# Kernel tuning notes

Hardware: AMD Instinct MI355X
Metric: run time of the kernel (lower is better)

## Reference

```python
import jax, jax.numpy as jnp
import numpy as np

B, S, D, H, FF = 2, 2048, 1024, 16, 4096
DK = D // H
EPS = 1e-5


def setup_inputs() -> dict:
    key = jax.random.key(0)
    ks = jax.random.split(key, 16)
    sd = 0.02
    return {
        "x": jax.random.normal(ks[0], (B, S, D), jnp.float32),
        "mask": jnp.ones((B, 1, 1, S), jnp.int32),
        "wq_w": jax.random.normal(ks[1], (D, D), jnp.float32) * sd,
        "wq_b": jnp.zeros((D,), jnp.float32),
        "wk_w": jax.random.normal(ks[2], (D, D), jnp.float32) * sd,
        "wk_b": jnp.zeros((D,), jnp.float32),
        "wv_w": jax.random.normal(ks[3], (D, D), jnp.float32) * sd,
        "wv_b": jnp.zeros((D,), jnp.float32),
        "wo_w": jax.random.normal(ks[4], (D, D), jnp.float32) * sd,
        "wo_b": jnp.zeros((D,), jnp.float32),
        "ff1_w": jax.random.normal(ks[5], (FF, D), jnp.float32) * sd,
        "ff1_b": jnp.zeros((FF,), jnp.float32),
        "ff2_w": jax.random.normal(ks[6], (D, FF), jnp.float32) * sd,
        "ff2_b": jnp.zeros((D,), jnp.float32),
        "ln1_a": jnp.ones((D,), jnp.float32),
        "ln1_b": jnp.zeros((D,), jnp.float32),
        "ln2_a": jnp.ones((D,), jnp.float32),
        "ln2_b": jnp.zeros((D,), jnp.float32),
    }


def _layernorm(x, alpha, beta):
    # Matches torch module: std is unbiased (ddof=1), divides by (std + eps)
    mean = jnp.mean(x, -1, keepdims=True)
    std = jnp.std(x, -1, keepdims=True, ddof=1)
    return (x - mean) / (std + EPS) * alpha + beta


def _mha(x, mask, wq_w, wq_b, wk_w, wk_b, wv_w, wv_b, wo_w, wo_b):
    q = (x @ wq_w.T + wq_b).reshape(B, S, H, DK).transpose(0, 2, 1, 3)
    k = (x @ wk_w.T + wk_b).reshape(B, S, H, DK).transpose(0, 2, 1, 3)
    v = (x @ wv_w.T + wv_b).reshape(B, S, H, DK).transpose(0, 2, 1, 3)
    scores = jnp.einsum('bhqd,bhkd->bhqk', q, k) / jnp.sqrt(jnp.float32(DK))
    scores = jnp.where(mask == 0, -jnp.inf, scores)
    attn = jax.nn.softmax(scores, axis=-1)
    out = jnp.einsum('bhqk,bhkd->bhqd', attn, v)
    out = out.transpose(0, 2, 1, 3).reshape(B, S, D)
    return out @ wo_w.T + wo_b


def reference(x, mask, wq_w, wq_b, wk_w, wk_b, wv_w, wv_b, wo_w, wo_b,
              ff1_w, ff1_b, ff2_w, ff2_b, ln1_a, ln1_b, ln2_a, ln2_b):
    # Residual 1: pre-norm + self-attention (dropout = 0)
    h = _layernorm(x, ln1_a, ln1_b)
    x = x + _mha(h, mask, wq_w, wq_b, wk_w, wk_b, wv_w, wv_b, wo_w, wo_b)
    # Residual 2: pre-norm + FFN
    h = _layernorm(x, ln2_a, ln2_b)
    ff = jax.nn.relu(h @ ff1_w.T + ff1_b) @ ff2_w.T + ff2_b
    return x + ff
```

## Files before the change

### kernel.cpp

```cpp
#include <hip/hip_runtime.h>
#include <hip/hip_bf16.h>
#include <stdint.h>

#define B_   2
#define S_   2048
#define D_   1024
#define H_   16
#define FF_  4096
#define TOK  4096
#define EPS_ 1e-5f
#define SC2  0.18033688f

typedef __attribute__((ext_vector_type(8))) short short8;
typedef __attribute__((ext_vector_type(4))) short short4_t;
typedef __attribute__((ext_vector_type(4))) float float4_t;

__device__ __forceinline__ short f2bf(float f) {
  union { float f; uint32_t u; } v; v.f = f;
  uint32_t r = v.u + 0x7fffu + ((v.u >> 16) & 1u);
  return (short)(r >> 16);
}

__device__ __forceinline__ float bf2f(short s) {
  union { uint32_t u; float f; } v; v.u = ((uint32_t)(uint16_t)s) << 16; return v.f;
}

__device__ __forceinline__ uint32_t pkbf(float a, float b) {
  __hip_bfloat162 h = __float22bfloat162_rn(make_float2(a, b));
  union { __hip_bfloat162 h; uint32_t u; } c; c.h = h; return c.u;
}

__device__ __forceinline__ void gload_lds16(const void* g, void* l) {
  __builtin_amdgcn_global_load_lds(
      (const __attribute__((address_space(1))) void*)g,
      (__attribute__((address_space(3))) void*)l, 16, 0, 0);
}

__global__ __launch_bounds__(256) void prep_kernel(
    const float* __restrict__ x, const float* __restrict__ ln1a,
    const float* __restrict__ ln1b, short* __restrict__ h1,
    const int* __restrict__ m, float* __restrict__ maskb, int* __restrict__ flags,
    const float* __restrict__ wq, const float* __restrict__ wk,
    const float* __restrict__ wv, const float* __restrict__ wo,
    const float* __restrict__ f1, const float* __restrict__ f2,
    short* __restrict__ wout)
{
  const int blk = blockIdx.x;
  const int tid = threadIdx.x;
  if (blk < TOK) {
    const int row = blk;
    const float4_t v = *(const float4_t*)(x + (size_t)row * D_ + tid * 4);
    float s  = v[0] + v[1] + v[2] + v[3];
    float ss = v[0]*v[0] + v[1]*v[1] + v[2]*v[2] + v[3]*v[3];
    #pragma unroll
    for (int mm = 1; mm < 64; mm <<= 1) { s += __shfl_xor(s, mm); ss += __shfl_xor(ss, mm); }
    __shared__ float red[8];
    const int wave = tid >> 6, lane = tid & 63;
    if (lane == 0) { red[wave] = s; red[4 + wave] = ss; }
    __syncthreads();
    s  = red[0] + red[1] + red[2] + red[3];
    ss = red[4] + red[5] + red[6] + red[7];
    const float mean = s * (1.0f / D_);
    float var = (ss - (float)D_ * mean * mean) * (1.0f / (D_ - 1));
    var = fmaxf(var, 0.0f);
    const float inv = 1.0f / (sqrtf(var) + EPS_);
    short4_t o;
    #pragma unroll
    for (int j = 0; j < 4; j++) {
      float a = ln1a[tid*4 + j], bb = ln1b[tid*4 + j];
      o[j] = f2bf((v[j] - mean) * inv * a + bb);
    }
    *(short4_t*)(h1 + (size_t)row * D_ + tid * 4) = o;
  } else if (blk < TOK + 16) {
    const int i = (blk - TOK) * 256 + tid;
    const int mv = m[i];
    maskb[i] = mv ? 0.0f : -1e30f;
    unsigned long long bal = __ballot(mv == 0);
    if ((tid & 63) == 0) flags[i >> 6] = (bal != 0ull) ? 1 : 0;
  } else {
    const int n4 = (12 << 20) / 4;
    const int nb = gridDim.x - TOK - 16;
    int idx = (blk - TOK - 16) * 256 + tid;
    const int stride = nb * 256;
    for (int j4 = idx; j4 < n4; j4 += stride) {
      const int j = j4 * 4;
      const int seg = j >> 20;
      const float* src; int off;
      if (seg < 4)      { src = (seg == 0) ? wq : (seg == 1) ? wk : (seg == 2) ? wv : wo;
                          off = j & ((1 << 20) - 1); }
      else if (seg < 8) { src = f1; off = j - (4 << 20); }
      else              { src = f2; off = j - (8 << 20); }
      float4_t v = *(const float4_t*)(src + off);
      short4_t o = { f2bf(v[0]), f2bf(v[1]), f2bf(v[2]), f2bf(v[3]) };
      *(short4_t*)(wout + j) = o;
    }
  }
}

__global__ void combine3_kernel(const float* __restrict__ x2,
                                const short* __restrict__ pA,
                                const short* __restrict__ pB,
                                float* __restrict__ out, const float* __restrict__ bias,
                                int n) {
  int idx = blockIdx.x * blockDim.x + threadIdx.x;
  int stride = gridDim.x * blockDim.x;
  for (int j = idx * 4; j < n; j += stride * 4) {
    float4_t a  = *(const float4_t*)(x2 + j);
    float4_t c  = *(const float4_t*)(out + j);
    float4_t bb = *(const float4_t*)(bias + (j & (D_ - 1)));
    short4_t q0 = *(const short4_t*)(pA + j);
    short4_t q1 = *(const short4_t*)(pA + (4u << 20) + j);
    short4_t q2 = *(const short4_t*)(pB + j);
    float4_t o;
    #pragma unroll
    for (int e = 0; e < 4; e++)
      o[e] = a[e] + c[e] + bb[e] + bf2f(q0[e]) + bf2f(q1[e]) + bf2f(q2[e]);
    *(float4_t*)(out + j) = o;
  }
}

__global__ __launch_bounds__(256) void ln_kernel(
    const float* __restrict__ x, const float* __restrict__ alpha,
    const float* __restrict__ beta, short* __restrict__ out)
{
  const int row = blockIdx.x;
  const int tid = threadIdx.x;
  const float4_t v = *(const float4_t*)(x + (size_t)row * D_ + tid * 4);
  float s  = v[0] + v[1] + v[2] + v[3];
  float ss = v[0]*v[0] + v[1]*v[1] + v[2]*v[2] + v[3]*v[3];
  #pragma unroll
  for (int m = 1; m < 64; m <<= 1) { s += __shfl_xor(s, m); ss += __shfl_xor(ss, m); }
  __shared__ float red[8];
  const int wave = tid >> 6, lane = tid & 63;
  if (lane == 0) { red[wave] = s; red[4 + wave] = ss; }
  __syncthreads();
  s  = red[0] + red[1] + red[2] + red[3];
  ss = red[4] + red[5] + red[6] + red[7];
  const float mean = s * (1.0f / D_);
  float var = (ss - (float)D_ * mean * mean) * (1.0f / (D_ - 1));
  var = fmaxf(var, 0.0f);
  const float inv = 1.0f / (sqrtf(var) + EPS_);
  short4_t o;
  #pragma unroll
  for (int j = 0; j < 4; j++) {
    float a = alpha[tid*4 + j], bb = beta[tid*4 + j];
    o[j] = f2bf((v[j] - mean) * inv * a + bb);
  }
  *(short4_t*)(out + (size_t)row * D_ + tid * 4) = o;
}

template<int EPI, int BN>
__global__ __launch_bounds__(256) void gemm_bt(
    const short* __restrict__ A, const short* __restrict__ Bm,
    void* __restrict__ Cout, void* __restrict__ Cout2,
    const float* __restrict__ bias, const float* __restrict__ res,
    int N, int K, int lda, int ldb)
{
  __shared__ __align__(16) short As[2][128][32];
  __shared__ __align__(16) short Bs[2][BN][32];

  const int tid  = threadIdx.x;
  const int wave = tid >> 6, lane = tid & 63;
  const int l15  = lane & 15, l4 = lane >> 4;

  const int gx = gridDim.x, gy = gridDim.y;
  int bid = (blockIdx.z * gy + blockIdx.y) * gx + blockIdx.x;
  const int q8 = (gx * gy * gridDim.z) >> 3;
  bid = (bid & 7) * q8 + (bid >> 3);
  const int n0 = (bid % gx) * BN;
  const int m0 = ((bid / gx) % gy) * 128;
  const int zi = bid / (gx * gy);
  const int koff = zi * K;

  constexpr int MI = (BN == 128) ? 4 : 2;
  const int rb = (BN == 128) ? (wave >> 1) * 64 : wave * 32;
  const int cb = (BN == 128) ? (wave & 1) * 64 : 0;

  float4_t acc[MI][4] = {};

  const int scol = (lane & 3) * 8;
  const short* gA0 = A + (size_t)(m0 + wave*32 + (lane >> 2)) * lda + koff + scol;
  const short* gA1 = gA0 + (size_t)16 * lda;
  const short* gB0;
  const short* gB1 = nullptr;
  if (BN == 128) {
    gB0 = Bm + (size_t)(n0 + wave*32 + (lane >> 2)) * ldb + koff + scol;
    gB1 = gB0 + (size_t)16 * ldb;
  } else {
    gB0 = Bm + (size_t)(n0 + wave*16 + (lane >> 2)) * ldb + koff + scol;
  }

  gload_lds16(gA0, &As[0][wave*32][0]);
  gload_lds16(gA1, &As[0][wave*32 + 16][0]);
  if (BN == 128) {
    gload_lds16(gB0, &Bs[0][wave*32][0]);
    gload_lds16(gB1, &Bs[0][wave*32 + 16][0]);
  } else {
    gload_lds16(gB0, &Bs[0][wave*16][0]);
  }

  for (int k0 = 0; k0 < K; k0 += 32) {
    const int cur = (k0 >> 5) & 1;
    __syncthreads();
    if (k0 + 32 < K) {
      gload_lds16(gA0 + k0 + 32, &As[cur^1][wave*32][0]);
      gload_lds16(gA1 + k0 + 32, &As[cur^1][wave*32 + 16][0]);
      if (BN == 128) {
        gload_lds16(gB0 + k0 + 32, &Bs[cur^1][wave*32][0]);
        gload_lds16(gB1 + k0 + 32, &Bs[cur^1][wave*32 + 16][0]);
      } else {
        gload_lds16(gB0 + k0 + 32, &Bs[cur^1][wave*16][0]);
      }
    }
    short8 af[MI], bf[4];
    #pragma unroll
    for (int i = 0; i < MI; i++)
      af[i] = *(const short8*)&As[cur][rb + i*16 + l15][l4*8];
    #pragma unroll
    for (int i = 0; i < 4; i++)
      bf[i] = *(const short8*)&Bs[cur][cb + i*16 + l15][l4*8];
    #pragma unroll
    for (int mi = 0; mi < MI; mi++)
      #pragma unroll
      for (int ni = 0; ni < 4; ni++)
        acc[mi][ni] = __builtin_amdgcn_mfma_f32_16x16x32_bf16(af[mi], bf[ni], acc[mi][ni], 0, 0, 0);
  }

  const int crow0 = m0 + rb + l4*4;
  const int ccol0 = n0 + cb + l15;
  #pragma unroll
  for (int mi = 0; mi < MI; mi++) {
    #pragma unroll
    for (int ni = 0; ni < 4; ni++) {
      const int col = ccol0 + ni*16;
      const float bc = bias[col];
      #pragma unroll
      for (int r = 0; r < 4; r++) {
        const int row = crow0 + mi*16 + r;
        ((float*)Cout)[(size_t)row * N + col] =
            res[(size_t)row * N + col] + acc[mi][ni][r] + bc;
      }
    }
  }
}

#define G256_DECLS                                                            \
  const int tid = threadIdx.x;                                                \
  const int w = tid >> 6, lane = tid & 63;                                    \
  const int wm = w >> 2, wn = w & 3;                                          \
  const int l15 = lane & 15, l4 = lane >> 4;                                  \
  const int srow = w*8 + (lane >> 3);                                         \
  const int schk = ((lane & 7) ^ (((lane >> 5) & 1) << 1)) * 8;               \
  const int rswz = (l4 ^ (((l15 >> 2) & 1) << 1)) * 8;                        \
  const int aoff = (wm*128 + l15) * 64 + rswz;                                \
  const int boff = (wn*64  + l15) * 64 + rswz;

#define G256_STG(buf_, koff_, LDA_) do {                                      \
    short* da = lds + (buf_)*16384 + w*512;                                   \
    short* db = lds + 32768 + (buf_)*16384 + w*512;                           \
    const short* sa = gA + (koff_);                                           \
    const short* sb = gB + (koff_);                                           \
    gload_lds16(sa,                      da);                                 \
    gload_lds16(sa +  64*(size_t)(LDA_), da + 4096);                          \
    gload_lds16(sa + 128*(size_t)(LDA_), da + 8192);                          \
    gload_lds16(sa + 192*(size_t)(LDA_), da + 12288);                         \
    gload_lds16(sb,                      db);                                 \
    gload_lds16(sb +  64*(size_t)(LDA_), db + 4096);                          \
    gload_lds16(sb + 128*(size_t)(LDA_), db + 8192);                          \
    gload_lds16(sb + 192*(size_t)(LDA_), db + 12288);                         \
  } while (0)

#define G256_LOOP(LDA_)                                                       \
  float4_t acc[8][4] = {};                                                    \
  G256_STG(0, 0, LDA_);                                                       \
  G256_STG(1, 64, LDA_);                                                      \
  for (int t = 0; t < 16; ++t) {                                              \
    const int cur = t & 1;                                                    \
    if (t < 15) asm volatile("s_waitcnt vmcnt(8)" ::: "memory");              \
    else        asm volatile("s_waitcnt vmcnt(0)" ::: "memory");              \
    __builtin_amdgcn_s_barrier();                                             \
    __builtin_amdgcn_sched_barrier(0);                                        \
    const short* La = lds + cur*16384 + aoff;                                 \
    const short* Lb = lds + 32768 + cur*16384 + boff;                         \
    short8 af[4][2], bf0[2][2], bf1[2][2];                                    \
    _Pragma("unroll") for (int mf = 0; mf < 4; mf++)                          \
      _Pragma("unroll") for (int ks = 0; ks < 2; ks++)                        \
        af[mf][ks] = *(const short8*)(La + mf*1024 + ks*32);                  \
    _Pragma("unroll") for (int nf = 0; nf < 2; nf++)                          \
      _Pragma("unroll") for (int ks = 0; ks < 2; ks++)                        \
        bf0[nf][ks] = *(const short8*)(Lb + nf*1024 + ks*32);                 \
    _Pragma("unroll") for (int nf = 0; nf < 2; nf++)                          \
      _Pragma("unroll") for (int ks = 0; ks < 2; ks++)                        \
        bf1[nf][ks] = *(const short8*)(Lb + (2+nf)*1024 + ks*32);             \
    __builtin_amdgcn_s_setprio(1);                                            \
    _Pragma("unroll") for (int mf = 0; mf < 4; mf++)                          \
      _Pragma("unroll") for (int nf = 0; nf < 2; nf++)                        \
        _Pragma("unroll") for (int ks = 0; ks < 2; ks++)                      \
          acc[mf][nf] = __builtin_amdgcn_mfma_f32_16x16x32_bf16(              \
              af[mf][ks], bf0[nf][ks], acc[mf][nf], 0, 0, 0);                 \
    __builtin_amdgcn_s_setprio(0);                                            \
    short8 a2[4][2];                                                          \
    _Pragma("unroll") for (int mf = 0; mf < 4; mf++)                          \
      _Pragma("unroll") for (int ks = 0; ks < 2; ks++)                        \
        a2[mf][ks] = *(const short8*)(La + (4+mf)*1024 + ks*32);              \
    __builtin_amdgcn_s_setprio(1);                                            \
    _Pragma("unroll") for (int mf = 0; mf < 4; mf++)                          \
      _Pragma("unroll") for (int nf = 0; nf < 2; nf++)                        \
        _Pragma("unroll") for (int ks = 0; ks < 2; ks++)                      \
          acc[mf][2+nf] = __builtin_amdgcn_mfma_f32_16x16x32_bf16(            \
              af[mf][ks], bf1[nf][ks], acc[mf][2+nf], 0, 0, 0);               \
    _Pragma("unroll") for (int mf = 0; mf < 4; mf++)                          \
      _Pragma("unroll") for (int nf = 0; nf < 2; nf++)                        \
        _Pragma("unroll") for (int ks = 0; ks < 2; ks++)                      \
          acc[4+mf][2+nf] = __builtin_amdgcn_mfma_f32_16x16x32_bf16(          \
              a2[mf][ks], bf1[nf][ks], acc[4+mf][2+nf], 0, 0, 0);             \
    __builtin_amdgcn_s_setprio(0);                                            \
    __builtin_amdgcn_s_barrier();        \
    if (t < 14) G256_STG(cur, (t+2)*64, LDA_);                                \
    __builtin_amdgcn_s_setprio(1);                                            \
    _Pragma("unroll") for (int mf = 0; mf < 4; mf++)                          \
      _Pragma("unroll") for (int nf = 0; nf < 2; nf++)                        \
        _Pragma("unroll") for (int ks = 0; ks < 2; ks++)                      \
          acc[4+mf][nf] = __builtin_amdgcn_mfma_f32_16x16x32_bf16(            \
              a2[mf][ks], bf0[nf][ks], acc[4+mf][nf], 0, 0, 0);               \
    __builtin_amdgcn_s_setprio(0);                                            \
  }

__global__ __launch_bounds__(512, 2) void ff1_256(
    const short* __restrict__ A, const short* __restrict__ Bm,
    short* __restrict__ Cout, const float* __restrict__ bias)
{
  __shared__ __align__(16) short lds[65536];
  G256_DECLS
  const int gx = gridDim.x;
  int bid = blockIdx.y * gx + blockIdx.x;
  const int q8 = (gx * gridDim.y) >> 3;
  bid = (bid & 7) * q8 + (bid >> 3);
  const int n0 = (bid % gx) * 256;
  const int m0 = (bid / gx) * 256;
  const short* gA = A  + (size_t)(m0 + srow) * 1024 + schk;
  const short* gB = Bm + (size_t)(n0 + srow) * 1024 + schk;

  G256_LOOP(1024)

  #pragma unroll
  for (int mf = 0; mf < 8; mf++) {
    #pragma unroll
    for (int nf = 0; nf < 4; nf++) {
      const int col = n0 + wn*64 + nf*16 + l15;
      const float bc = bias[col];
      #pragma unroll
      for (int r = 0; r < 4; r++) {
        const int row = m0 + wm*128 + mf*16 + l4*4 + r;
        Cout[(size_t)row * FF_ + col] = f2bf(fmaxf(acc[mf][nf][r] + bc, 0.0f));
      }
    }
  }
}

__global__ __launch_bounds__(512, 2) void qkv_256(
    const short* __restrict__ A, const short* __restrict__ Bm,
    short* __restrict__ qkbuf, short* __restrict__ vt,
    const float* __restrict__ qb, const float* __restrict__ kb,
    const float* __restrict__ vb)
{
  __shared__ __align__(16) short lds[65536];
  G256_DECLS
  const int gx = gridDim.x;
  int bid = blockIdx.y * gx + blockIdx.x;
  const int q8 = (gx * gridDim.y) >> 3;
  bid = (bid & 7) * q8 + (bid >> 3);
  const int n0 = (bid % gx) * 256;
  const int m0 = (bid / gx) * 256;
  const short* gA = A  + (size_t)(m0 + srow) * 1024 + schk;
  const short* gB = Bm + (size_t)(n0 + srow) * 1024 + schk;

  G256_LOOP(1024)

  const int seg = n0 >> 10;
  if (seg < 2) {
    const float* bb = seg ? kb : qb;
    const float scl = seg ? 1.0f : SC2;
    #pragma unroll
    for (int mf = 0; mf < 8; mf++)
      #pragma unroll
      for (int nf = 0; nf < 4; nf++) {
        const int col = n0 + wn*64 + nf*16 + l15;
        const float bc = bb[col & 1023];
        #pragma unroll
        for (int r = 0; r < 4; r++) {
          const int row = m0 + wm*128 + mf*16 + l4*4 + r;
          qkbuf[(size_t)row * 2048 + col] = f2bf((acc[mf][nf][r] + bc) * scl);
        }
      }
  } else {
    #pragma unroll
    for (int mf = 0; mf < 8; mf++)
      #pragma unroll
      for (int nf = 0; nf < 4; nf++) {
        const int d = n0 + wn*64 + nf*16 + l15 - 2048;
        const float bc = vb[d];
        const int row0 = m0 + wm*128 + mf*16 + l4*4;
        short4_t o = { f2bf(acc[mf][nf][0] + bc), f2bf(acc[mf][nf][1] + bc),
                       f2bf(acc[mf][nf][2] + bc), f2bf(acc[mf][nf][3] + bc) };
        *(short4_t*)&vt[(size_t)d * TOK + row0] = o;
      }
  }
}

__global__ __launch_bounds__(512, 2) void ff2_256(
    const short* __restrict__ A, const short* __restrict__ Bm,
    short* __restrict__ pA, short* __restrict__ pB, float* __restrict__ dout)
{
  __shared__ __align__(16) short lds[65536];
  G256_DECLS
  const int gx = gridDim.x, gy = gridDim.y;
  int bid = (blockIdx.z * gy + blockIdx.y) * gx + blockIdx.x;
  const int q8 = (gx * gy * gridDim.z) >> 3;
  bid = (bid & 7) * q8 + (bid >> 3);
  const int n0 = (bid % gx) * 256;
  const int m0 = ((bid / gx) % gy) * 256;
  const int zi = bid / (gx * gy);
  const short* gA = A  + (size_t)(m0 + srow) * 4096 + zi*1024 + schk;
  const short* gB = Bm + (size_t)(n0 + srow) * 4096 + zi*1024 + schk;

  G256_LOOP(4096)

  if (zi < 3) {
    short* dst = (zi < 2) ? (pA + (size_t)zi * (4u << 20)) : pB;
    #pragma unroll
    for (int mf = 0; mf < 8; mf++)
      #pragma unroll
      for (int nf = 0; nf < 4; nf++) {
        const int col = n0 + wn*64 + nf*16 + l15;
        #pragma unroll
        for (int r = 0; r < 4; r++) {
          const int row = m0 + wm*128 + mf*16 + l4*4 + r;
          dst[(size_t)row * D_ + col] = f2bf(acc[mf][nf][r]);
        }
      }
  } else {
    #pragma unroll
    for (int mf = 0; mf < 8; mf++)
      #pragma unroll
      for (int nf = 0; nf < 4; nf++) {
        const int col = n0 + wn*64 + nf*16 + l15;
        #pragma unroll
        for (int r = 0; r < 4; r++) {
          const int row = m0 + wm*128 + mf*16 + l4*4 + r;
          dout[(size_t)row * D_ + col] = acc[mf][nf][r];
        }
      }
  }
}

__global__ __launch_bounds__(256, 4) void attn_kernel(
    const short* __restrict__ qk, const short* __restrict__ vt,
    const float* __restrict__ maskb, const int* __restrict__ mflags,
    short* __restrict__ out)
{
  int bid = (blockIdx.z * H_ + blockIdx.y) * (S_/64) + blockIdx.x;
  bid = (bid & 7) * ((B_ * H_ * (S_/64)) >> 3) + (bid >> 3);
  const int qt = bid % (S_/64);
  const int h  = (bid / (S_/64)) % H_;
  const int b  = bid / ((S_/64) * H_);

  const int tid = threadIdx.x, wave = tid >> 6, lane = tid & 63;
  const int l15 = lane & 15, l4 = lane >> 4;
  const int q0 = qt * 64 + wave * 16;

  __shared__ __align__(16) short Kt[2][4096];
  __shared__ __align__(16) short Vt[2][4096];

  short8 qa[2];
  #pragma unroll
  for (int kc = 0; kc < 2; kc++)
    qa[kc] = *(const short8*)&qk[(size_t)(b*S_ + q0 + l15) * 2048 + h*64 + kc*32 + l4*8];

  short8 ones;
  #pragma unroll
  for (int i = 0; i < 8; i++) ones[i] = (short)0x3F80;

  float4_t acc[4];
  #pragma unroll
  for (int dg = 0; dg < 4; dg++) acc[dg] = (float4_t){0.f, 0.f, 0.f, 0.f};
  float4_t accl = (float4_t){0.f, 0.f, 0.f, 0.f};
  float m2 = 0.0f;

  const int r8 = lane >> 3;
  const int ch = (lane & 7) ^ ((r8 & 3) | ((wave & 1) << 2));
  const int sbase = wave * 512;

  #pragma unroll
  for (int i = 0; i < 2; i++) {
    const int row = i*32 + wave*8 + r8;
    gload_lds16(qk + (size_t)(b*S_ + row) * 2048 + 1024 + h*64 + ch*8, &Kt[0][sbase + i*2048]);
    gload_lds16(vt + (size_t)(h*64 + row) * TOK + b*S_ + ch*8,         &Vt[0][sbase + i*2048]);
  }

  int krow[4];
  #pragma unroll
  for (int kg = 0; kg < 4; kg++)
    krow[kg] = 32*(kg>>1) + 8*(l15>>2) + 4*(kg&1) + (l15&3);
  const int gq = (l15 & 3) | (((l15 >> 2) & 1) << 2);
  const int gv = (l15 & 3) | (((l15 >> 3) & 1) << 2);

  for (int t = 0; t < S_/64; t++) {
    const int cur = t & 1;
    __syncthreads();
    if (t + 1 < S_/64) {
      const int k1 = (t + 1) * 64;
      #pragma unroll
      for (int i = 0; i < 2; i++) {
        const int row = i*32 + wave*8 + r8;
        gload_lds16(qk + (size_t)(b*S_ + k1 + row) * 2048 + 1024 + h*64 + ch*8, &Kt[cur^1][sbase + i*2048]);
        gload_lds16(vt + (size_t)(h*64 + row) * TOK + b*S_ + k1 + ch*8,         &Vt[cur^1][sbase + i*2048]);
      }
    }
    const short* Kc = &Kt[cur][0];
    const short* Vc = &Vt[cur][0];

    short8 kf[4][2], vf[4][2];
    #pragma unroll
    for (int kg = 0; kg < 4; kg++)
      #pragma unroll
      for (int kc = 0; kc < 2; kc++)
        kf[kg][kc] = *(const short8*)(Kc + krow[kg]*64 + ((l4 + kc*4) ^ gq) * 8);
    #pragma unroll
    for (int dg = 0; dg < 4; dg++)
      #pragma unroll
      for (int pc = 0; pc < 2; pc++)
        vf[dg][pc] = *(const short8*)(Vc + (dg*16 + l15)*64 + ((l4 + pc*4) ^ gv) * 8);

    const float negm2 = -m2;
    float4_t sc[4];
    #pragma unroll
    for (int kg = 0; kg < 4; kg++)
      sc[kg] = (float4_t){negm2, negm2, negm2, negm2};
    __builtin_amdgcn_s_setprio(1);
    #pragma unroll
    for (int kg = 0; kg < 4; kg++)
      #pragma unroll
      for (int kc = 0; kc < 2; kc++)
        sc[kg] = __builtin_amdgcn_mfma_f32_16x16x32_bf16(kf[kg][kc], qa[kc], sc[kg], 0, 0, 0);
    __builtin_amdgcn_s_setprio(0);

    if (mflags[b*(S_/64) + t]) {
      #pragma unroll
      for (int kg = 0; kg < 4; kg++) {
        float4_t mb = *(const float4_t*)&maskb[b*S_ + t*64 + 32*(kg>>1) + 4*(kg&1) + 8*l4];
        #pragma unroll
        for (int r = 0; r < 4; r++) sc[kg][r] += mb[r];
      }
    }

    float pm = fmaxf(fmaxf(sc[0][0], sc[0][1]), sc[0][2]);
    pm = fmaxf(fmaxf(pm, sc[0][3]), sc[1][0]);
    pm = fmaxf(fmaxf(pm, sc[1][1]), sc[1][2]);
    pm = fmaxf(fmaxf(pm, sc[1][3]), sc[2][0]);
    pm = fmaxf(fmaxf(pm, sc[2][1]), sc[2][2]);
    pm = fmaxf(fmaxf(pm, sc[2][3]), sc[3][0]);
    pm = fmaxf(fmaxf(pm, sc[3][1]), sc[3][2]);
    pm = fmaxf(pm, sc[3][3]);
    pm = fmaxf(pm, __shfl_xor(pm, 16));
    pm = fmaxf(pm, __shfl_xor(pm, 32));
    if (__any(pm > 8.0f)) {
      const float shift = fmaxf(pm, 0.0f);
      m2 += shift;
      const float esc = exp2f(-shift);
      #pragma unroll
      for (int r = 0; r < 4; r++) {
        const float er = __shfl(esc, l4*4 + r);
        #pragma unroll
        for (int dg = 0; dg < 4; dg++) acc[dg][r] *= er;
        accl[r] *= er;
      }
      #pragma unroll
      for (int kg = 0; kg < 4; kg++)
        #pragma unroll
        for (int r = 0; r < 4; r++) sc[kg][r] -= shift;
    }
    #pragma unroll
    for (int kg = 0; kg < 4; kg++)
      #pragma unroll
      for (int r = 0; r < 4; r++)
        sc[kg][r] = exp2f(sc[kg][r]);

    union { short8 s8; uint32_t u[4]; } pu[2];
    #pragma unroll
    for (int pc = 0; pc < 2; pc++) {
      pu[pc].u[0] = pkbf(sc[2*pc][0],   sc[2*pc][1]);
      pu[pc].u[1] = pkbf(sc[2*pc][2],   sc[2*pc][3]);
      pu[pc].u[2] = pkbf(sc[2*pc+1][0], sc[2*pc+1][1]);
      pu[pc].u[3] = pkbf(sc[2*pc+1][2], sc[2*pc+1][3]);
    }
    __builtin_amdgcn_s_setprio(1);
    #pragma unroll
    for (int dg = 0; dg < 4; dg++)
      #pragma unroll
      for (int pc = 0; pc < 2; pc++)
        acc[dg] = __builtin_amdgcn_mfma_f32_16x16x32_bf16(pu[pc].s8, vf[dg][pc], acc[dg], 0, 0, 0);
    #pragma unroll
    for (int pc = 0; pc < 2; pc++)
      accl = __builtin_amdgcn_mfma_f32_16x16x32_bf16(pu[pc].s8, ones, accl, 0, 0, 0);
    __builtin_amdgcn_s_setprio(0);
  }

  float linv[4];
  #pragma unroll
  for (int r = 0; r < 4; r++) linv[r] = 1.0f / accl[r];
  #pragma unroll
  for (int dg = 0; dg < 4; dg++)
    #pragma unroll
    for (int r = 0; r < 4; r++)
      out[(size_t)(b*S_ + q0 + l4*4 + r) * D_ + h*64 + dg*16 + l15] =
          f2bf(acc[dg][r] * linv[r]);
}

extern "C" void kernel_launch(void* const* d_in, const int* in_sizes, int n_in,
                              void* d_out, int out_size, void* d_ws, size_t ws_size,
                              hipStream_t stream)
{
  const float* x     = (const float*)d_in[0];
  const int*   mask  = (const int*)d_in[1];
  const float* wq_w  = (const float*)d_in[2];
  const float* wq_b  = (const float*)d_in[3];
  const float* wk_w  = (const float*)d_in[4];
  const float* wk_b  = (const float*)d_in[5];
  const float* wv_w  = (const float*)d_in[6];
  const float* wv_b  = (const float*)d_in[7];
  const float* wo_w  = (const float*)d_in[8];
  const float* wo_b  = (const float*)d_in[9];
  const float* ff1_w = (const float*)d_in[10];
  const float* ff1_b = (const float*)d_in[11];
  const float* ff2_w = (const float*)d_in[12];
  const float* ff2_b = (const float*)d_in[13];
  const float* ln1_a = (const float*)d_in[14];
  const float* ln1_b = (const float*)d_in[15];
  const float* ln2_a = (const float*)d_in[16];
  const float* ln2_b = (const float*)d_in[17];

  uint8_t* ws = (uint8_t*)d_ws;
  const size_t MB = 1024 * 1024;
  short* wqkv  = (short*)(ws + 0);
  short* wob   = (short*)(ws + 6*MB);
  short* ff1b  = (short*)(ws + 8*MB);
  short* ff2b  = (short*)(ws + 16*MB);
  float* maskb = (float*)(ws + 24*MB + 64*1024);
  int*   mflg  = (int*)(ws + 24*MB + 128*1024);
  short* h1    = (short*)(ws + 25*MB);
  short* attno = (short*)(ws + 25*MB);
  short* pB    = (short*)(ws + 25*MB);
  short* qkbuf = (short*)(ws + 33*MB);
  short* vt    = (short*)(ws + 49*MB);
  float* x2    = (float*)(ws + 65*MB);
  short* ffa   = (short*)(ws + 33*MB);
  short* pA    = (short*)(ws + 0);

  prep_kernel<<<TOK + 16 + 1536, 256, 0, stream>>>(
      x, ln1_a, ln1_b, h1, mask, maskb, mflg,
      wq_w, wk_w, wv_w, wo_w, ff1_w, ff2_w, (short*)ws);
  qkv_256<<<dim3(3072/256, TOK/256), 512, 0, stream>>>(
      h1, wqkv, qkbuf, vt, wq_b, wk_b, wv_b);
  attn_kernel<<<dim3(S_/64, H_, B_), 256, 0, stream>>>(qkbuf, vt, maskb, mflg, attno);
  gemm_bt<3,64><<<dim3(1024/64, TOK/128), 256, 0, stream>>>(
      attno, wob, x2, nullptr, wo_b, x, 1024, 1024, 1024, 1024);
  ln_kernel<<<TOK, 256, 0, stream>>>(x2, ln2_a, ln2_b, h1);
  ff1_256<<<dim3(FF_/256, TOK/256), 512, 0, stream>>>(h1, ff1b, ffa, ff1_b);
  ff2_256<<<dim3(1024/256, TOK/256, 4), 512, 0, stream>>>(
      ffa, ff2b, pA, pB, (float*)d_out);
  combine3_kernel<<<2048, 256, 0, stream>>>(x2, pA, pB, (float*)d_out, ff2_b, TOK * D_);
}
```

Before: 241.1 us.

## Replace output-projection GEMM with split-K 256-tile kernel and fused LN2 reduction

The output projection moves from a small 128x64-tile GEMM to the 256x256 tiled MFMA pipeline, using 4-way split-K that writes bf16 partials. The second layernorm kernel now sums the four partials with the residual and bias, writes x2, and normalizes in one pass. This aims to raise MFMA efficiency and fill the GPU on the 1024x1024 projection. In exchange it adds partial-buffer traffic and rounds each partial to bf16, which costs some precision.

```diff
diff --git a/kernel.cpp b/kernel.cpp
--- a/kernel.cpp
+++ b/kernel.cpp
@@ -119,13 +119,26 @@
   }
 }
 
-__global__ __launch_bounds__(256) void ln_kernel(
-    const float* __restrict__ x, const float* __restrict__ alpha,
-    const float* __restrict__ beta, short* __restrict__ out)
+__global__ __launch_bounds__(256) void ln2f4_kernel(
+    const short* __restrict__ pW,
+    const float* __restrict__ x, const float* __restrict__ ob,
+    const float* __restrict__ alpha, const float* __restrict__ beta,
+    float* __restrict__ x2, short* __restrict__ h2)
 {
   const int row = blockIdx.x;
   const int tid = threadIdx.x;
-  const float4_t v = *(const float4_t*)(x + (size_t)row * D_ + tid * 4);
+  const size_t idx = (size_t)row * D_ + tid * 4;
+  float4_t a  = *(const float4_t*)(x + idx);
+  float4_t bb = *(const float4_t*)(ob + tid * 4);
+  short4_t p0 = *(const short4_t*)(pW + idx);
+  short4_t p1 = *(const short4_t*)(pW + (size_t)1*(4u<<20) + idx);
+  short4_t p2 = *(const short4_t*)(pW + (size_t)2*(4u<<20) + idx);
+  short4_t p3 = *(const short4_t*)(pW + (size_t)3*(4u<<20) + idx);
+  float4_t v;
+  #pragma unroll
+  for (int e = 0; e < 4; e++)
+    v[e] = a[e] + bb[e] + bf2f(p0[e]) + bf2f(p1[e]) + bf2f(p2[e]) + bf2f(p3[e]);
+  *(float4_t*)(x2 + idx) = v;
   float s  = v[0] + v[1] + v[2] + v[3];
   float ss = v[0]*v[0] + v[1]*v[1] + v[2]*v[2] + v[3]*v[3];
   #pragma unroll
@@ -143,105 +156,10 @@
   short4_t o;
   #pragma unroll
   for (int j = 0; j < 4; j++) {
-    float a = alpha[tid*4 + j], bb = beta[tid*4 + j];
-    o[j] = f2bf((v[j] - mean) * inv * a + bb);
-  }
-  *(short4_t*)(out + (size_t)row * D_ + tid * 4) = o;
-}
-
-template<int EPI, int BN>
-__global__ __launch_bounds__(256) void gemm_bt(
-    const short* __restrict__ A, const short* __restrict__ Bm,
-    void* __restrict__ Cout, void* __restrict__ Cout2,
-    const float* __restrict__ bias, const float* __restrict__ res,
-    int N, int K, int lda, int ldb)
-{
-  __shared__ __align__(16) short As[2][128][32];
-  __shared__ __align__(16) short Bs[2][BN][32];
-
-  const int tid  = threadIdx.x;
-  const int wave = tid >> 6, lane = tid & 63;
-  const int l15  = lane & 15, l4 = lane >> 4;
-
-  const int gx = gridDim.x, gy = gridDim.y;
-  int bid = (blockIdx.z * gy + blockIdx.y) * gx + blockIdx.x;
-  const int q8 = (gx * gy * gridDim.z) >> 3;
-  bid = (bid & 7) * q8 + (bid >> 3);
-  const int n0 = (bid % gx) * BN;
-  const int m0 = ((bid / gx) % gy) * 128;
-  const int zi = bid / (gx * gy);
-  const int koff = zi * K;
-
-  constexpr int MI = (BN == 128) ? 4 : 2;
-  const int rb = (BN == 128) ? (wave >> 1) * 64 : wave * 32;
-  const int cb = (BN == 128) ? (wave & 1) * 64 : 0;
-
-  float4_t acc[MI][4] = {};
-
-  const int scol = (lane & 3) * 8;
-  const short* gA0 = A + (size_t)(m0 + wave*32 + (lane >> 2)) * lda + koff + scol;
-  const short* gA1 = gA0 + (size_t)16 * lda;
-  const short* gB0;
-  const short* gB1 = nullptr;
-  if (BN == 128) {
-    gB0 = Bm + (size_t)(n0 + wave*32 + (lane >> 2)) * ldb + koff + scol;
-    gB1 = gB0 + (size_t)16 * ldb;
-  } else {
-    gB0 = Bm + (size_t)(n0 + wave*16 + (lane >> 2)) * ldb + koff + scol;
-  }
-
-  gload_lds16(gA0, &As[0][wave*32][0]);
-  gload_lds16(gA1, &As[0][wave*32 + 16][0]);
-  if (BN == 128) {
-    gload_lds16(gB0, &Bs[0][wave*32][0]);
-    gload_lds16(gB1, &Bs[0][wave*32 + 16][0]);
-  } else {
-    gload_lds16(gB0, &Bs[0][wave*16][0]);
-  }
-
-  for (int k0 = 0; k0 < K; k0 += 32) {
-    const int cur = (k0 >> 5) & 1;
-    __syncthreads();
-    if (k0 + 32 < K) {
-      gload_lds16(gA0 + k0 + 32, &As[cur^1][wave*32][0]);
-      gload_lds16(gA1 + k0 + 32, &As[cur^1][wave*32 + 16][0]);
-      if (BN == 128) {
-        gload_lds16(gB0 + k0 + 32, &Bs[cur^1][wave*32][0]);
-        gload_lds16(gB1 + k0 + 32, &Bs[cur^1][wave*32 + 16][0]);
-      } else {
-        gload_lds16(gB0 + k0 + 32, &Bs[cur^1][wave*16][0]);
-      }
-    }
-    short8 af[MI], bf[4];
-    #pragma unroll
-    for (int i = 0; i < MI; i++)
-      af[i] = *(const short8*)&As[cur][rb + i*16 + l15][l4*8];
-    #pragma unroll
-    for (int i = 0; i < 4; i++)
-      bf[i] = *(const short8*)&Bs[cur][cb + i*16 + l15][l4*8];
-    #pragma unroll
-    for (int mi = 0; mi < MI; mi++)
-      #pragma unroll
-      for (int ni = 0; ni < 4; ni++)
-        acc[mi][ni] = __builtin_amdgcn_mfma_f32_16x16x32_bf16(af[mi], bf[ni], acc[mi][ni], 0, 0, 0);
-  }
-
-  const int crow0 = m0 + rb + l4*4;
-  const int ccol0 = n0 + cb + l15;
-  #pragma unroll
-  for (int mi = 0; mi < MI; mi++) {
-    #pragma unroll
-    for (int ni = 0; ni < 4; ni++) {
-      const int col = ccol0 + ni*16;
-      const float bc = bias[col];
-      #pragma unroll
-      for (int r = 0; r < 4; r++) {
-        const int row = crow0 + mi*16 + r;
-        ((float*)Cout)[(size_t)row * N + col] =
-            res[(size_t)row * N + col] + acc[mi][ni][r] + bc;
-      }
-    }
-  }
+    float al = alpha[tid*4 + j], be = beta[tid*4 + j];
+    o[j] = f2bf((v[j] - mean) * inv * al + be);
+  }
+  *(short4_t*)(h2 + idx) = o;
 }
 
 #define G256_DECLS                                                            \
@@ -270,14 +188,14 @@
     gload_lds16(sb + 192*(size_t)(LDA_), db + 12288);                         \
   } while (0)
 
-#define G256_LOOP(LDA_)                                                       \
+#define G256_LOOP(LDA_, NT_)                                                  \
   float4_t acc[8][4] = {};                                                    \
   G256_STG(0, 0, LDA_);                                                       \
   G256_STG(1, 64, LDA_);                                                      \
-  for (int t = 0; t < 16; ++t) {                                              \
+  for (int t = 0; t < (NT_); ++t) {                                           \
     const int cur = t & 1;                                                    \
-    if (t < 15) asm volatile("s_waitcnt vmcnt(8)" ::: "memory");              \
-    else        asm volatile("s_waitcnt vmcnt(0)" ::: "memory");              \
+    if (t < (NT_) - 1) asm volatile("s_waitcnt vmcnt(8)" ::: "memory");       \
+    else               asm volatile("s_waitcnt vmcnt(0)" ::: "memory");       \
     __builtin_amdgcn_s_barrier();                                             \
     __builtin_amdgcn_sched_barrier(0);                                        \
     const short* La = lds + cur*16384 + aoff;                                 \
@@ -316,7 +234,7 @@
               a2[mf][ks], bf1[nf][ks], acc[4+mf][2+nf], 0, 0, 0);             \
     __builtin_amdgcn_s_setprio(0);                                            \
     __builtin_amdgcn_s_barrier();        \
-    if (t < 14) G256_STG(cur, (t+2)*64, LDA_);                                \
+    if (t < (NT_) - 2) G256_STG(cur, (t+2)*64, LDA_);                         \
     __builtin_amdgcn_s_setprio(1);                                            \
     _Pragma("unroll") for (int mf = 0; mf < 4; mf++)                          \
       _Pragma("unroll") for (int nf = 0; nf < 2; nf++)                        \
@@ -341,7 +259,7 @@
   const short* gA = A  + (size_t)(m0 + srow) * 1024 + schk;
   const short* gB = Bm + (size_t)(n0 + srow) * 1024 + schk;
 
-  G256_LOOP(1024)
+  G256_LOOP(1024, 16)
 
   #pragma unroll
   for (int mf = 0; mf < 8; mf++) {
@@ -375,7 +293,7 @@
   const short* gA = A  + (size_t)(m0 + srow) * 1024 + schk;
   const short* gB = Bm + (size_t)(n0 + srow) * 1024 + schk;
 
-  G256_LOOP(1024)
+  G256_LOOP(1024, 16)
 
   const int seg = n0 >> 10;
   if (seg < 2) {
@@ -424,7 +342,7 @@
   const short* gA = A  + (size_t)(m0 + srow) * 4096 + zi*1024 + schk;
   const short* gB = Bm + (size_t)(n0 + srow) * 4096 + zi*1024 + schk;
 
-  G256_LOOP(4096)
+  G256_LOOP(4096, 16)
 
   if (zi < 3) {
     short* dst = (zi < 2) ? (pA + (size_t)zi * (4u << 20)) : pB;
@@ -452,6 +370,38 @@
         }
       }
   }
+}
+
+__global__ __launch_bounds__(512, 2) void wo_256(
+    const short* __restrict__ A, const short* __restrict__ Bm,
+    short* __restrict__ pW)
+{
+  __shared__ __align__(16) short lds[65536];
+  G256_DECLS
+  const int gx = gridDim.x, gy = gridDim.y;
+  int bid = (blockIdx.z * gy + blockIdx.y) * gx + blockIdx.x;
+  const int q8 = (gx * gy * gridDim.z) >> 3;
+  bid = (bid & 7) * q8 + (bid >> 3);
+  const int n0 = (bid % gx) * 256;
+  const int m0 = ((bid / gx) % gy) * 256;
+  const int zi = bid / (gx * gy);
+  const short* gA = A  + (size_t)(m0 + srow) * 1024 + zi*256 + schk;
+  const short* gB = Bm + (size_t)(n0 + srow) * 1024 + zi*256 + schk;
+
+  G256_LOOP(1024, 4)
+
+  short* dst = pW + (size_t)zi * (4u << 20);
+  #pragma unroll
+  for (int mf = 0; mf < 8; mf++)
+    #pragma unroll
+    for (int nf = 0; nf < 4; nf++) {
+      const int col = n0 + wn*64 + nf*16 + l15;
+      #pragma unroll
+      for (int r = 0; r < 4; r++) {
+        const int row = m0 + wm*128 + mf*16 + l4*4 + r;
+        dst[(size_t)row * D_ + col] = f2bf(acc[mf][nf][r]);
+      }
+    }
 }
 
 __global__ __launch_bounds__(256, 4) void attn_kernel(
@@ -653,6 +603,7 @@
   short* pB    = (short*)(ws + 25*MB);
   short* qkbuf = (short*)(ws + 33*MB);
   short* vt    = (short*)(ws + 49*MB);
+  short* pW    = (short*)(ws + 33*MB);
   float* x2    = (float*)(ws + 65*MB);
   short* ffa   = (short*)(ws + 33*MB);
   short* pA    = (short*)(ws + 0);
@@ -663,9 +614,8 @@
   qkv_256<<<dim3(3072/256, TOK/256), 512, 0, stream>>>(
       h1, wqkv, qkbuf, vt, wq_b, wk_b, wv_b);
   attn_kernel<<<dim3(S_/64, H_, B_), 256, 0, stream>>>(qkbuf, vt, maskb, mflg, attno);
-  gemm_bt<3,64><<<dim3(1024/64, TOK/128), 256, 0, stream>>>(
-      attno, wob, x2, nullptr, wo_b, x, 1024, 1024, 1024, 1024);
-  ln_kernel<<<TOK, 256, 0, stream>>>(x2, ln2_a, ln2_b, h1);
+  wo_256<<<dim3(1024/256, TOK/256, 4), 512, 0, stream>>>(attno, wob, pW);
+  ln2f4_kernel<<<TOK, 256, 0, stream>>>(pW, x, wo_b, ln2_a, ln2_b, x2, h1);
   ff1_256<<<dim3(FF_/256, TOK/256), 512, 0, stream>>>(h1, ff1b, ffa, ff1_b);
   ff2_256<<<dim3(1024/256, TOK/256, 4), 512, 0, stream>>>(
       ffa, ff2b, pA, pB, (float*)d_out);
```

Result: slower. 247.1 us (+2.5%).
